# Performance work log

Hardware: AMD Instinct MI355X
Metric: run time of the kernel (lower is better)

## Reference

```python
import jax, jax.numpy as jnp
import numpy as np

B, N, D, H = 16, 1024, 384, 6
DH = D // H  # 64 per-head dim


def _layernorm(x, w, b, eps=1e-5):
    mu = jnp.mean(x, axis=-1, keepdims=True)
    var = jnp.var(x, axis=-1, keepdims=True)
    return (x - mu) * jax.lax.rsqrt(var + eps) * w + b


def setup_inputs() -> dict:
    key = jax.random.key(0)
    ks = jax.random.split(key, 10)
    std = 0.02
    return {
        "X": jax.random.normal(ks[0], (B, N, D), dtype=jnp.float32),
        "Wq": jax.random.normal(ks[1], (H, DH, D), dtype=jnp.float32) * std,
        "Wk": jax.random.normal(ks[2], (H, DH, D), dtype=jnp.float32) * std,
        "Wv": jax.random.normal(ks[3], (H, DH, D), dtype=jnp.float32) * std,
        "Wo": jax.random.normal(ks[4], (D, D), dtype=jnp.float32) * std,
        "bo": jnp.zeros((D,), dtype=jnp.float32),
        "ln1_w": jnp.ones((D,), dtype=jnp.float32),
        "ln1_b": jnp.zeros((D,), dtype=jnp.float32),
        "ln2_w": jnp.ones((D,), dtype=jnp.float32),
        "ln2_b": jnp.zeros((D,), dtype=jnp.float32),
        "W1": jax.random.normal(ks[5], (2 * D, D), dtype=jnp.float32) * std,
        "b1": jnp.zeros((2 * D,), dtype=jnp.float32),
        "W2": jax.random.normal(ks[6], (D, 2 * D), dtype=jnp.float32) * std,
        "b2": jnp.zeros((D,), dtype=jnp.float32),
    }


def reference(X, Wq, Wk, Wv, Wo, bo, ln1_w, ln1_b, ln2_w, ln2_b, W1, b1, W2, b2):
    scale = 1.0 / jnp.sqrt(jnp.float32(DH))
    # pre-LN then multi-head attention (heads vectorized, math identical to per-head loop)
    t = _layernorm(X, ln1_w, ln1_b)                       # [B,N,D]
    q = jnp.einsum('bnd,hkd->bhnk', t, Wq)                # [B,H,N,DH]
    k = jnp.einsum('bnd,hkd->bhnk', t, Wk)
    v = jnp.einsum('bnd,hkd->bhnk', t, Wv)
    scores = jnp.einsum('bhnk,bhmk->bhnm', q, k) * scale  # [B,H,N,N]
    p = jax.nn.softmax(scores, axis=-1)
    o = jnp.einsum('bhnm,bhmk->bhnk', p, v)               # [B,H,N,DH]
    o = jnp.transpose(o, (0, 2, 1, 3)).reshape(B, N, D)   # concat heads
    attn = o @ Wo.T + bo
    # residual + post-LN (dropout/drop_path are identity in eval)
    X2 = _layernorm(X + attn, ln2_w, ln2_b)
    # MLP: Linear -> exact GELU -> Linear
    h = jax.nn.gelu(X2 @ W1.T + b1, approximate=False)
    mlp = h @ W2.T + b2
    return X2 + mlp
```

## Files before the change

### kernel.cpp

```cpp
#include <hip/hip_runtime.h>
#include <math.h>

typedef float  f32x4  __attribute__((ext_vector_type(4)));
typedef __bf16 bf16x8 __attribute__((ext_vector_type(8)));
typedef __bf16 bf16x4 __attribute__((ext_vector_type(4)));

__device__ __forceinline__ void gload16(const void* g, void* l) {
  __builtin_amdgcn_global_load_lds((__attribute__((address_space(1))) const void*)g,
                                   (__attribute__((address_space(3))) void*)l, 16, 0, 0);
}

__device__ __forceinline__ f32x4 mfma16(bf16x8 a, bf16x8 b, f32x4 c) {
  return __builtin_amdgcn_mfma_f32_16x16x32_bf16(a, b, c, 0, 0, 0);
}

__global__ __launch_bounds__(256) void cvt_weights(
    const float* __restrict__ Wq, const float* __restrict__ Wk, const float* __restrict__ Wv,
    const float* __restrict__ Wo, const float* __restrict__ W1, const float* __restrict__ W2,
    __bf16* __restrict__ wqkv, __bf16* __restrict__ wo, __bf16* __restrict__ w1, __bf16* __restrict__ w2)
{
  const int idx = (blockIdx.x * 256 + threadIdx.x) * 4;
  const float* src; __bf16* dst; int off;
  if      (idx < 147456) { src = Wq; dst = wqkv;          off = idx; }
  else if (idx < 294912) { src = Wk; dst = wqkv + 147456; off = idx - 147456; }
  else if (idx < 442368) { src = Wv; dst = wqkv + 294912; off = idx - 294912; }
  else if (idx < 589824) { src = Wo; dst = wo;            off = idx - 442368; }
  else if (idx < 884736) { src = W1; dst = w1;            off = idx - 589824; }
  else                   { src = W2; dst = w2;            off = idx - 884736; }
  f32x4 v = *(const f32x4*)(src + off);
  bf16x4 o = {(__bf16)v.x, (__bf16)v.y, (__bf16)v.z, (__bf16)v.w};
  *(bf16x4*)(dst + off) = o;
}

template<int MODE>
__global__ __launch_bounds__(256) void ln_kernel(
    const float* __restrict__ in, const float* __restrict__ w, const float* __restrict__ b,
    __bf16* __restrict__ outb, float* __restrict__ outf)
{
  const int row  = blockIdx.x * 4 + (threadIdx.x >> 6);
  const int lane = threadIdx.x & 63;
  const float* x = in + (size_t)row * 384;
  float v[6]; float s = 0.f;
#pragma unroll
  for (int j = 0; j < 6; ++j) { v[j] = x[lane + 64*j]; s += v[j]; }
#pragma unroll
  for (int off = 32; off > 0; off >>= 1) s += __shfl_xor(s, off);
  const float mu = s * (1.f/384.f);
  float s2 = 0.f;
#pragma unroll
  for (int j = 0; j < 6; ++j) { float d = v[j] - mu; s2 += d*d; }
#pragma unroll
  for (int off = 32; off > 0; off >>= 1) s2 += __shfl_xor(s2, off);
  const float inv = rsqrtf(s2 * (1.f/384.f) + 1e-5f);
#pragma unroll
  for (int j = 0; j < 6; ++j) {
    const int cidx = lane + 64*j;
    const float y = (v[j]-mu)*inv*w[cidx] + b[cidx];
    outb[(size_t)row*384 + cidx] = (__bf16)y;
    if constexpr (MODE == 1) outf[(size_t)row*384 + cidx] = y;
  }
}

template<int EPI, int NT>
__global__ __launch_bounds__(256, NT == 128 ? 3 : 4) void gemm_bt(
    const __bf16* __restrict__ A, const __bf16* __restrict__ Bw,
    int M, int N, int K,
    const float* __restrict__ bias, const float* __restrict__ resid,
    float* __restrict__ outf, __bf16* __restrict__ outb,
    __bf16* __restrict__ q_out, __bf16* __restrict__ k_out, __bf16* __restrict__ vt_out)
{
  constexpr int CT     = NT / 32;
  constexpr int BSUB   = NT / 16;
  constexpr int ROUNDS = (8 + BSUB) / 4;
  __shared__ __attribute__((aligned(16))) __bf16 As[2][4096];
  __shared__ __attribute__((aligned(16))) __bf16 Bs[2][NT * 32];
  const int tid  = threadIdx.x;
  const int lane = tid & 63;
  const int w    = tid >> 6;
  const int wm   = w >> 1, wn = w & 1;
  const int m0   = blockIdx.y * 128, n0 = blockIdx.x * NT;

  f32x4 acc[4][CT] = {};

  const int srow = lane & 15, skq = lane >> 4;
  const __bf16* gptr[ROUNDS];
  __bf16*       lptr[ROUNDS];
  int           lstr[ROUNDS];
#pragma unroll
  for (int r = 0; r < ROUNDS; ++r) {
    const int id = r * 4 + w;
    if (id < 8) {
      gptr[r] = A + (size_t)(m0 + id*16 + srow) * K + (skq << 3);
      lptr[r] = &As[0][id * 512];
      lstr[r] = 4096;
    } else {
      const int j = id - 8;
      gptr[r] = Bw + (size_t)(n0 + j*16 + srow) * K + (skq << 3);
      lptr[r] = &Bs[0][j * 512];
      lstr[r] = NT * 32;
    }
  }

  auto stage = [&](int kk, int b) {
#pragma unroll
    for (int r = 0; r < ROUNDS; ++r)
      gload16(gptr[r] + kk * 32, lptr[r] + b * lstr[r]);
  };
  auto compute = [&](int b) {
    bf16x8 af[4], bfr[CT];
#pragma unroll
    for (int i = 0; i < 4; ++i)
      af[i] = *(const bf16x8*)&As[b][(wm*4 + i) * 512 + lane * 8];
#pragma unroll
    for (int j = 0; j < CT; ++j)
      bfr[j] = *(const bf16x8*)&Bs[b][(wn*CT + j) * 512 + lane * 8];
#pragma unroll
    for (int i = 0; i < 4; ++i)
#pragma unroll
      for (int j = 0; j < CT; ++j)
        acc[i][j] = mfma16(af[i], bfr[j], acc[i][j]);
  };

  const int NIT = K >> 5;
  stage(0, 0);
  __syncthreads();
  for (int k = 0; k < NIT; ++k) {
    const int b = k & 1;
    if (k + 1 < NIT) stage(k + 1, b ^ 1);
    compute(b);
    __syncthreads();
  }

  const int quad = lane >> 4, cc = lane & 15;
#pragma unroll
  for (int rt = 0; rt < 4; ++rt) {
#pragma unroll
    for (int ct = 0; ct < CT; ++ct) {
      const int gr0 = m0 + (wm*4 + rt)*16 + quad*4;
      const int gc  = n0 + (wn*CT + ct)*16 + cc;
      f32x4 a = acc[rt][ct];
      if constexpr (EPI == 0) {
        const int bb = gr0 >> 10, nn = gr0 & 1023;
        if (gc >= 768) {
          const int jj = gc - 768, hh = jj >> 6, dh = jj & 63;
          bf16x4 pk = {(__bf16)a[0], (__bf16)a[1], (__bf16)a[2], (__bf16)a[3]};
          *(bf16x4*)&vt_out[((size_t)((bb*6 + hh)*64 + dh) << 10) + nn] = pk;
        } else {
          const bool isq = (gc < 384);
          const int jj = isq ? gc : (gc - 384);
          __bf16* dst = isq ? q_out : k_out;
          const float sc = isq ? 0.18033688011112042f : 1.0f;
          const int hh = jj >> 6, dh = jj & 63;
#pragma unroll
          for (int i = 0; i < 4; ++i)
            dst[((size_t)(((bb*6 + hh) << 10) | (nn + i)) << 6) + dh] = (__bf16)(a[i] * sc);
        }
      } else {
#pragma unroll
        for (int i = 0; i < 4; ++i) {
          const int gr = gr0 + i;
          float val = a[i];
          if constexpr (EPI == 1) {
            const size_t idx = (size_t)gr * N + gc;
            outf[idx] = val + bias[gc] + resid[idx];
          } else if constexpr (EPI == 2) {
            const float x = val + bias[gc];
            outb[(size_t)gr * N + gc] = (__bf16)(0.5f * x * (1.f + erff(x * 0.70710678118654752f)));
          } else {
            const size_t idx = (size_t)gr * N + gc;
            outf[idx] = outf[idx] + val + bias[gc];
          }
        }
      }
    }
  }
}

__global__ __launch_bounds__(256, 3) void attn_kernel(
    const __bf16* __restrict__ qp, const __bf16* __restrict__ kp,
    const __bf16* __restrict__ vtp, __bf16* __restrict__ omat)
{
  __shared__ __attribute__((aligned(16))) __bf16 Ks[2][4096];
  __shared__ __attribute__((aligned(16))) __bf16 Vs[2][4096];
  __shared__ __attribute__((aligned(16))) __bf16 Ps[4][2][1088];
  const int tid = threadIdx.x, lane = tid & 63, w = tid >> 6;
  const int bh = blockIdx.x;
  const int q0 = blockIdx.y * 128 + w * 32;
  const int quad = lane >> 4, lo = lane & 15;

  bf16x8 qa[2][2];
#pragma unroll
  for (int t = 0; t < 2; ++t) {
    const __bf16* qb = qp + ((size_t)bh * 1024 + q0 + t*16 + lo) * 64 + (quad << 3);
    qa[t][0] = *(const bf16x8*)qb;
    qa[t][1] = *(const bf16x8*)(qb + 32);
  }

  f32x4 oacc[2][4] = {};
  float l_r[2] = {0.f, 0.f};

  auto stage = [&](int c, int bb) {
#pragma unroll
    for (int s = 0; s < 2; ++s) {
      const int ck = s * 256 + tid;
      const int l = ck & 63, g = ck >> 6;
      const int ct = g >> 1, ks = g & 1;
      const __bf16* gk = kp + ((size_t)bh*1024 + c*64 + ct*16 + (l & 15)) * 64
                            + ks*32 + ((l >> 4) << 3);
      gload16(gk, &Ks[bb][(ck & ~63) * 8]);
      const __bf16* gv = vtp + (((size_t)(bh*64 + ct*16 + (l & 15))) << 10)
                             + c*64 + ks*32 + ((l >> 4) << 3);
      gload16(gv, &Vs[bb][(ck & ~63) * 8]);
    }
  };

  stage(0, 0);
  __syncthreads();

  for (int c = 0; c < 16; ++c) {
    const int bb = c & 1;
    if (c + 1 < 16) stage(c + 1, bb ^ 1);

    f32x4 st[2][4];
#pragma unroll
    for (int ct = 0; ct < 4; ++ct) {
      bf16x8 kb0 = *(const bf16x8*)&Ks[bb][((ct*2 + 0)*64 + lane) * 8];
      bf16x8 kb1 = *(const bf16x8*)&Ks[bb][((ct*2 + 1)*64 + lane) * 8];
#pragma unroll
      for (int t = 0; t < 2; ++t) {
        f32x4 s0 = {};
        s0 = mfma16(kb0, qa[t][0], s0);
        s0 = mfma16(kb1, qa[t][1], s0);
        st[t][ct] = s0;
      }
    }
#pragma unroll
    for (int t = 0; t < 2; ++t)
#pragma unroll
      for (int ct = 0; ct < 4; ++ct) {
        const float p0 = __builtin_amdgcn_exp2f(st[t][ct][0]);
        const float p1 = __builtin_amdgcn_exp2f(st[t][ct][1]);
        const float p2 = __builtin_amdgcn_exp2f(st[t][ct][2]);
        const float p3 = __builtin_amdgcn_exp2f(st[t][ct][3]);
        l_r[t] += (p0 + p1) + (p2 + p3);
        bf16x4 pk = {(__bf16)p0, (__bf16)p1, (__bf16)p2, (__bf16)p3};
        *(bf16x4*)&Ps[w][t][lo*68 + ct*16 + quad*4] = pk;
      }
    bf16x8 pa[2][2];
#pragma unroll
    for (int t = 0; t < 2; ++t)
#pragma unroll
      for (int ks = 0; ks < 2; ++ks)
        pa[t][ks] = *(const bf16x8*)&Ps[w][t][lo*68 + ks*32 + (quad << 3)];
#pragma unroll
    for (int dt = 0; dt < 4; ++dt)
#pragma unroll
      for (int ks = 0; ks < 2; ++ks) {
        bf16x8 vb = *(const bf16x8*)&Vs[bb][((dt*2 + ks)*64 + lane) * 8];
#pragma unroll
        for (int t = 0; t < 2; ++t)
          oacc[t][dt] = mfma16(pa[t][ks], vb, oacc[t][dt]);
      }
    __syncthreads();
  }

  const int b = bh / 6, h = bh - (bh / 6) * 6;
#pragma unroll
  for (int t = 0; t < 2; ++t) {
    float ls = l_r[t];
    ls += __shfl_xor(ls, 16);
    ls += __shfl_xor(ls, 32);
#pragma unroll
    for (int i = 0; i < 4; ++i) {
      const float linv = 1.f / __shfl(ls, quad*4 + i);
      const int n = q0 + t*16 + quad*4 + i;
#pragma unroll
      for (int dt = 0; dt < 4; ++dt)
        omat[((size_t)((b << 10) | n)) * 384 + (h << 6) + dt*16 + lo] =
            (__bf16)(oacc[t][dt][i] * linv);
    }
  }
}

extern "C" void kernel_launch(void* const* d_in, const int* in_sizes, int n_in,
                              void* d_out, int out_size, void* d_ws, size_t ws_size,
                              hipStream_t stream)
{
  const float* X    = (const float*)d_in[0];
  const float* Wq   = (const float*)d_in[1];
  const float* Wk   = (const float*)d_in[2];
  const float* Wv   = (const float*)d_in[3];
  const float* Wo   = (const float*)d_in[4];
  const float* bo   = (const float*)d_in[5];
  const float* ln1w = (const float*)d_in[6];
  const float* ln1b = (const float*)d_in[7];
  const float* ln2w = (const float*)d_in[8];
  const float* ln2b = (const float*)d_in[9];
  const float* W1   = (const float*)d_in[10];
  const float* b1   = (const float*)d_in[11];
  const float* W2   = (const float*)d_in[12];
  const float* b2   = (const float*)d_in[13];

  char* ws = (char*)d_ws;
  __bf16* t_bf  = (__bf16*)(ws + 0);
  __bf16* q_bf  = (__bf16*)(ws + 12582912);
  __bf16* k_bf  = (__bf16*)(ws + 25165824);
  __bf16* omat  = (__bf16*)(ws + 37748736);
  __bf16* vt_bf = (__bf16*)(ws + 50331648);
  float*  s1    = (float*) (ws + 62914560);
  __bf16* h_bf  = (__bf16*)(ws + 62914560);
  __bf16* wqkv  = (__bf16*)(ws + 88080384);
  __bf16* wo_b  = (__bf16*)(ws + 88965120);
  __bf16* w1_b  = (__bf16*)(ws + 89260032);
  __bf16* w2_b  = (__bf16*)(ws + 89849856);
  __bf16* x2_bf = t_bf;
  float*  out   = (float*)d_out;

  cvt_weights<<<1152, 256, 0, stream>>>(Wq, Wk, Wv, Wo, W1, W2, wqkv, wo_b, w1_b, w2_b);
  ln_kernel<0><<<4096, 256, 0, stream>>>(X, ln1w, ln1b, t_bf, nullptr);
  gemm_bt<0,128><<<dim3(9,128), 256, 0, stream>>>(t_bf, wqkv, 16384, 1152, 384,
      nullptr, nullptr, nullptr, nullptr, q_bf, k_bf, vt_bf);
  attn_kernel<<<dim3(96,8), 256, 0, stream>>>(q_bf, k_bf, vt_bf, omat);
  gemm_bt<1,64><<<dim3(6,128), 256, 0, stream>>>(omat, wo_b, 16384, 384, 384,
      bo, X, s1, nullptr, nullptr, nullptr, nullptr);
  ln_kernel<1><<<4096, 256, 0, stream>>>(s1, ln2w, ln2b, x2_bf, out);
  gemm_bt<2,128><<<dim3(6,128), 256, 0, stream>>>(x2_bf, w1_b, 16384, 768, 384,
      b1, nullptr, nullptr, h_bf, nullptr, nullptr, nullptr);
  gemm_bt<3,64><<<dim3(6,128), 256, 0, stream>>>(h_bf, w2_b, 16384, 384, 768,
      b2, nullptr, out, nullptr, nullptr, nullptr, nullptr);
}
```

Measured before the change: 279.2 us.

## Deepen GEMM K-tile, swap grid axes, and use polynomial erf GELU

Adds a BK template parameter so three of the GEMMs stage 64-wide K slices per iteration, which halves the number of barriers and pipeline steps at the cost of more LDS and possibly lower occupancy. The grid is transposed so that consecutive blocks walk along M while sharing one weight tile, which is meant to improve L2 reuse of weights. The exact erff in the W1 GELU epilogue is replaced with an Abramowitz-Stegun polynomial using hardware rcp/exp2, which adds a small approximation error of roughly 1e-7, well below bf16 output precision.

```diff
diff --git a/kernel.cpp b/kernel.cpp
--- a/kernel.cpp
+++ b/kernel.cpp
@@ -12,6 +12,18 @@
 
 __device__ __forceinline__ f32x4 mfma16(bf16x8 a, bf16x8 b, f32x4 c) {
   return __builtin_amdgcn_mfma_f32_16x16x32_bf16(a, b, c, 0, 0, 0);
+}
+
+__device__ __forceinline__ float fast_gelu(float x) {
+  const float xs = x * 0.70710678118654752f;
+  const float ax = fabsf(xs);
+  const float t  = __builtin_amdgcn_rcpf(1.f + 0.3275911f * ax);
+  const float poly = ((((1.061405429f*t - 1.453152027f)*t + 1.421413741f)*t
+                       - 0.284496736f)*t + 0.254829592f)*t;
+  const float e = __builtin_amdgcn_exp2f(-1.4426950408889634f * ax * ax);
+  float erfv = 1.f - poly * e;
+  erfv = (xs < 0.f) ? -erfv : erfv;
+  return 0.5f * x * (1.f + erfv);
 }
 
 __global__ __launch_bounds__(256) void cvt_weights(
@@ -61,8 +73,8 @@
   }
 }
 
-template<int EPI, int NT>
-__global__ __launch_bounds__(256, NT == 128 ? 3 : 4) void gemm_bt(
+template<int EPI, int NT, int BK>
+__global__ __launch_bounds__(256, (NT == 128 && BK == 64) ? 2 : 3) void gemm_bt(
     const __bf16* __restrict__ A, const __bf16* __restrict__ Bw,
     int M, int N, int K,
     const float* __restrict__ bias, const float* __restrict__ resid,
@@ -70,15 +82,17 @@
     __bf16* __restrict__ q_out, __bf16* __restrict__ k_out, __bf16* __restrict__ vt_out)
 {
   constexpr int CT     = NT / 32;
-  constexpr int BSUB   = NT / 16;
-  constexpr int ROUNDS = (8 + BSUB) / 4;
-  __shared__ __attribute__((aligned(16))) __bf16 As[2][4096];
-  __shared__ __attribute__((aligned(16))) __bf16 Bs[2][NT * 32];
+  constexpr int KS     = BK / 32;
+  constexpr int ASUB   = 8 * KS;
+  constexpr int BSUB   = (NT / 16) * KS;
+  constexpr int ROUNDS = (ASUB + BSUB) / 4;
+  __shared__ __attribute__((aligned(16))) __bf16 As[2][4096 * KS];
+  __shared__ __attribute__((aligned(16))) __bf16 Bs[2][NT * 32 * KS];
   const int tid  = threadIdx.x;
   const int lane = tid & 63;
   const int w    = tid >> 6;
   const int wm   = w >> 1, wn = w & 1;
-  const int m0   = blockIdx.y * 128, n0 = blockIdx.x * NT;
+  const int m0   = blockIdx.x * 128, n0 = blockIdx.y * NT;
 
   f32x4 acc[4][CT] = {};
 
@@ -89,39 +103,43 @@
 #pragma unroll
   for (int r = 0; r < ROUNDS; ++r) {
     const int id = r * 4 + w;
-    if (id < 8) {
-      gptr[r] = A + (size_t)(m0 + id*16 + srow) * K + (skq << 3);
-      lptr[r] = &As[0][id * 512];
-      lstr[r] = 4096;
+    if (id < ASUB) {
+      const int ks = id >> 3, ms = id & 7;
+      gptr[r] = A + (size_t)(m0 + ms*16 + srow) * K + ks*32 + (skq << 3);
+      lptr[r] = &As[0][ks * 4096 + ms * 512];
+      lstr[r] = 4096 * KS;
     } else {
-      const int j = id - 8;
-      gptr[r] = Bw + (size_t)(n0 + j*16 + srow) * K + (skq << 3);
-      lptr[r] = &Bs[0][j * 512];
-      lstr[r] = NT * 32;
+      const int j = id - ASUB, ks = j / (NT/16), ns = j % (NT/16);
+      gptr[r] = Bw + (size_t)(n0 + ns*16 + srow) * K + ks*32 + (skq << 3);
+      lptr[r] = &Bs[0][ks * (NT*32) + ns * 512];
+      lstr[r] = NT * 32 * KS;
     }
   }
 
   auto stage = [&](int kk, int b) {
 #pragma unroll
     for (int r = 0; r < ROUNDS; ++r)
-      gload16(gptr[r] + kk * 32, lptr[r] + b * lstr[r]);
+      gload16(gptr[r] + kk * BK, lptr[r] + b * lstr[r]);
   };
   auto compute = [&](int b) {
-    bf16x8 af[4], bfr[CT];
-#pragma unroll
-    for (int i = 0; i < 4; ++i)
-      af[i] = *(const bf16x8*)&As[b][(wm*4 + i) * 512 + lane * 8];
-#pragma unroll
-    for (int j = 0; j < CT; ++j)
-      bfr[j] = *(const bf16x8*)&Bs[b][(wn*CT + j) * 512 + lane * 8];
-#pragma unroll
-    for (int i = 0; i < 4; ++i)
+#pragma unroll
+    for (int ks = 0; ks < KS; ++ks) {
+      bf16x8 af[4], bfr[CT];
+#pragma unroll
+      for (int i = 0; i < 4; ++i)
+        af[i] = *(const bf16x8*)&As[b][ks*4096 + (wm*4 + i)*512 + lane*8];
 #pragma unroll
       for (int j = 0; j < CT; ++j)
-        acc[i][j] = mfma16(af[i], bfr[j], acc[i][j]);
+        bfr[j] = *(const bf16x8*)&Bs[b][ks*(NT*32) + (wn*CT + j)*512 + lane*8];
+#pragma unroll
+      for (int i = 0; i < 4; ++i)
+#pragma unroll
+        for (int j = 0; j < CT; ++j)
+          acc[i][j] = mfma16(af[i], bfr[j], acc[i][j]);
+    }
   };
 
-  const int NIT = K >> 5;
+  const int NIT = K / BK;
   stage(0, 0);
   __syncthreads();
   for (int k = 0; k < NIT; ++k) {
@@ -164,8 +182,7 @@
             const size_t idx = (size_t)gr * N + gc;
             outf[idx] = val + bias[gc] + resid[idx];
           } else if constexpr (EPI == 2) {
-            const float x = val + bias[gc];
-            outb[(size_t)gr * N + gc] = (__bf16)(0.5f * x * (1.f + erff(x * 0.70710678118654752f)));
+            outb[(size_t)gr * N + gc] = (__bf16)fast_gelu(val + bias[gc]);
           } else {
             const size_t idx = (size_t)gr * N + gc;
             outf[idx] = outf[idx] + val + bias[gc];
@@ -318,14 +335,14 @@
 
   cvt_weights<<<1152, 256, 0, stream>>>(Wq, Wk, Wv, Wo, W1, W2, wqkv, wo_b, w1_b, w2_b);
   ln_kernel<0><<<4096, 256, 0, stream>>>(X, ln1w, ln1b, t_bf, nullptr);
-  gemm_bt<0,128><<<dim3(9,128), 256, 0, stream>>>(t_bf, wqkv, 16384, 1152, 384,
+  gemm_bt<0,128,32><<<dim3(128,9), 256, 0, stream>>>(t_bf, wqkv, 16384, 1152, 384,
       nullptr, nullptr, nullptr, nullptr, q_bf, k_bf, vt_bf);
   attn_kernel<<<dim3(96,8), 256, 0, stream>>>(q_bf, k_bf, vt_bf, omat);
-  gemm_bt<1,64><<<dim3(6,128), 256, 0, stream>>>(omat, wo_b, 16384, 384, 384,
+  gemm_bt<1,64,64><<<dim3(128,6), 256, 0, stream>>>(omat, wo_b, 16384, 384, 384,
       bo, X, s1, nullptr, nullptr, nullptr, nullptr);
   ln_kernel<1><<<4096, 256, 0, stream>>>(s1, ln2w, ln2b, x2_bf, out);
-  gemm_bt<2,128><<<dim3(6,128), 256, 0, stream>>>(x2_bf, w1_b, 16384, 768, 384,
+  gemm_bt<2,128,64><<<dim3(128,6), 256, 0, stream>>>(x2_bf, w1_b, 16384, 768, 384,
       b1, nullptr, nullptr, h_bf, nullptr, nullptr, nullptr);
-  gemm_bt<3,64><<<dim3(6,128), 256, 0, stream>>>(h_bf, w2_b, 16384, 384, 768,
+  gemm_bt<3,64,64><<<dim3(128,6), 256, 0, stream>>>(h_bf, w2_b, 16384, 384, 768,
       b2, nullptr, out, nullptr, nullptr, nullptr, nullptr);
 }
```

Measured after the change: 274.4 us. No clear change (-1.7%).
